# Kernel optimization log

Hardware: AMD Instinct MI355X
Metric: run time of the kernel (lower is better)

Reference implementation:

```python
import jax, jax.numpy as jnp
import numpy as np


def _layernorm(x, g, b, eps=1e-5):
    m = x.mean(-1, keepdims=True)
    v = ((x - m) ** 2).mean(-1, keepdims=True)
    return (x - m) * jax.lax.rsqrt(v + eps) * g + b


def setup_inputs() -> dict:
    key = jax.random.key(0)
    ks = jax.random.split(key, 12)
    B, V, E, N = 8, 64, 512, 32          # batch, num_vars, embed(=input_dim), num_samples
    L, H, D, M, R = 4, 8, 64, 1024, 128  # layers, heads, head_dim, mlp_dim, resolution
    HD = H * D
    s = 0.02
    return {
        "flow_encoded": jax.random.normal(ks[0], (B, V, E), jnp.float32),
        "W_shift": s * jax.random.normal(ks[1], (E, HD), jnp.float32),
        "b_shift": jnp.zeros((HD,), jnp.float32),
        "Wk": s * jax.random.normal(ks[2], (L, H, E, D), jnp.float32),
        "bk": jnp.zeros((L, H, D), jnp.float32),
        "Wv": s * jax.random.normal(ks[3], (L, H, E, D), jnp.float32),
        "bv": jnp.zeros((L, H, D), jnp.float32),
        "ln1_g": jnp.ones((L, HD), jnp.float32),
        "ln1_b": jnp.zeros((L, HD), jnp.float32),
        "W1": s * jax.random.normal(ks[4], (L, HD, M), jnp.float32),
        "b1": jnp.zeros((L, M), jnp.float32),
        "W2": s * jax.random.normal(ks[5], (L, M, M), jnp.float32),
        "b2": jnp.zeros((L, M), jnp.float32),
        "W3": s * jax.random.normal(ks[6], (L, M, HD), jnp.float32),
        "b3": jnp.zeros((L, HD), jnp.float32),
        "ln2_g": jnp.ones((L, HD), jnp.float32),
        "ln2_b": jnp.zeros((L, HD), jnp.float32),
        "W_dist": s * jax.random.normal(ks[7], (HD, R), jnp.float32),
        "b_dist": jnp.zeros((R,), jnp.float32),
        "num_samples": N,
    }


def _forward_logits(flow_encoded, W_shift, b_shift, Wk, bk, Wv, bv,
                    ln1_g, ln1_b, W1, b1, W2, b2, W3, b3, ln2_g, ln2_b,
                    W_dist, b_dist, num_samples):
    B, V, E = flow_encoded.shape
    L, H, _, D = Wk.shape
    HD = H * D
    # history keys/values: all heads in one einsum (replaces per-head nn.Linear loop)
    keys = jnp.einsum('bve,lhed->lbhvd', flow_encoded, Wk) + bk[:, None, :, None, :]
    vals = jnp.einsum('bve,lhed->lbhvd', flow_encoded, Wv) + bv[:, None, :, None, :]
    # queries per (var, sample); vectorized over vars (outer loop in source is independent)
    att = flow_encoded @ W_shift + b_shift                      # [B, V, HD]
    att = jnp.broadcast_to(att[:, :, None, :], (B, V, num_samples, HD))
    scale = D ** -0.5
    for l in range(L):
        q = att.reshape(B, V, num_samples, H, D)
        scores = jnp.einsum('bvnhd,bhwd->bvnhw', q, keys[l]) * scale
        w = jax.nn.softmax(scores, axis=-1)
        a = jnp.einsum('bvnhw,bhwd->bvnhd', w, vals[l]).reshape(B, V, num_samples, HD)
        att = _layernorm(att + a, ln1_g[l], ln1_b[l])
        h = jax.nn.relu(att @ W1[l] + b1[l])
        h = jax.nn.relu(h @ W2[l] + b2[l])
        h = h @ W3[l] + b3[l]
        att = _layernorm(att + h, ln2_g[l], ln2_b[l])
    return att @ W_dist + b_dist                                # [B, V, N, R]


def reference(flow_encoded, W_shift, b_shift, Wk, bk, Wv, bv,
              ln1_g, ln1_b, W1, b1, W2, b2, W3, b3, ln2_g, ln2_b,
              W_dist, b_dist, num_samples):
    logits = _forward_logits(flow_encoded, W_shift, b_shift, Wk, bk, Wv, bv,
                             ln1_g, ln1_b, W1, b1, W2, b2, W3, b3, ln2_g, ln2_b,
                             W_dist, b_dist, num_samples)
    R = b_dist.shape[0]
    k = jax.random.key(1)
    idx = jax.random.categorical(jax.random.fold_in(k, 0), logits, axis=-1)  # multinomial(1)
    u = jax.random.uniform(jax.random.fold_in(k, 1), idx.shape, jnp.float32)
    samples = (idx.astype(jnp.float32) + u) / R                 # [B, V, N]
    return samples
```

## Files before the change

### kernel.cpp

```cpp
#include <hip/hip_runtime.h>
#include <hip/hip_bf16.h>
#include <math.h>

constexpr int B  = 8,  V = 64, E = 512, NS = 32;
constexpr int L  = 4,  H = 8,  D = 64,  M  = 1024, R = 128;
constexpr int HD = H * D;
constexpr int ROWS  = B * V;
constexpr int SROWS = ROWS * NS;
constexpr int KVN = 4096;

typedef _Float16 half8 __attribute__((ext_vector_type(8)));
typedef float floatx4 __attribute__((ext_vector_type(4)));

struct TF2 { unsigned a, b; };
__host__ __device__ constexpr unsigned rotl32(unsigned x, int d) {
  return (x << d) | (x >> (32 - d));
}
__host__ __device__ constexpr TF2 threefry(unsigned k0, unsigned k1,
                                           unsigned x0, unsigned x1) {
  unsigned ks2 = k0 ^ k1 ^ 0x1BD11BDAu;
  x0 += k0; x1 += k1;
  const int ra[4] = {13, 15, 26, 6};
  const int rb[4] = {17, 29, 16, 24};
  for (int i = 0; i < 4; i++) { x0 += x1; x1 = rotl32(x1, ra[i]); x1 ^= x0; }
  x0 += k1;  x1 += ks2 + 1u;
  for (int i = 0; i < 4; i++) { x0 += x1; x1 = rotl32(x1, rb[i]); x1 ^= x0; }
  x0 += ks2; x1 += k0 + 2u;
  for (int i = 0; i < 4; i++) { x0 += x1; x1 = rotl32(x1, ra[i]); x1 ^= x0; }
  x0 += k0;  x1 += k1 + 3u;
  for (int i = 0; i < 4; i++) { x0 += x1; x1 = rotl32(x1, rb[i]); x1 ^= x0; }
  x0 += k1;  x1 += ks2 + 4u;
  for (int i = 0; i < 4; i++) { x0 += x1; x1 = rotl32(x1, ra[i]); x1 ^= x0; }
  x0 += ks2; x1 += k0 + 5u;
  return {x0, x1};
}
__device__ __forceinline__ unsigned tf_bits32(unsigned k0, unsigned k1,
                                              unsigned j) {
  TF2 r = threefry(k0, k1, 0u, j);
  return r.a ^ r.b;
}

__device__ __forceinline__ double waveReduceAdd64(double v) {
#pragma unroll
  for (int m = 32; m; m >>= 1) v += __shfl_xor(v, m, 64);
  return v;
}

__device__ __forceinline__ void split16(float v, _Float16& h, _Float16& l) {
  h = (_Float16)v;
  l = (_Float16)((v - (float)h) * 2048.0f);
}

struct WArgs {
  const float* s[7];
  _Float16* h[7];
  _Float16* l[7];
};
__global__ __launch_bounds__(256) void prep_split(
    WArgs a, const float* __restrict__ flow, const float* __restrict__ bk,
    const float* __restrict__ bv, const float* __restrict__ bsh,
    _Float16* __restrict__ fh, _Float16* __restrict__ fl,
    float* __restrict__ kvb) {
  __shared__ float tile[64][65];
  const int bid = blockIdx.x, t = threadIdx.x;
  if (bid < 275) {
    if (bid < 256) {
      const int base = (bid * 256 + t) * 4;
      float4 v = *(const float4*)&flow[base];
      float x[4] = {v.x, v.y, v.z, v.w};
#pragma unroll
      for (int j = 0; j < 4; j++) {
        _Float16 h, l;
        split16(x[j], h, l);
        fh[base + j] = h;
        fl[base + j] = l;
      }
    } else {
      const int idx = (bid - 256) * 256 + t;
      if (idx < KVN + HD) {
        float bb = (idx < 2048) ? bk[idx]
                 : (idx < 4096) ? bv[idx - 2048]
                                : bsh[idx - 4096];
        kvb[idx] = bb;
      }
    }
    return;
  }
  const int WS_OFF[8] = {0, 64, 320, 576, 1088, 2112, 2624, 2640};
  const int WS_K[7] = {512, 512, 512, 512, 1024, 1024, 512};
  const int WS_N[7] = {512, 64, 64, 1024, 1024, 512, 128};
  int wb = bid - 275;
  int mi = 0;
  while (wb >= WS_OFF[mi + 1]) mi++;
  int tt = wb - WS_OFF[mi];
  const int K = WS_K[mi], N = WS_N[mi];
  const int ktiles = K >> 6;
  const int per = ktiles * (N >> 6);
  const int z = tt / per;
  const int rem = tt - z * per;
  const int k0 = (rem % ktiles) * 64, n0 = (rem / ktiles) * 64;
  const size_t moff = (size_t)z * K * N;
  const float* src = a.s[mi] + moff;
  _Float16* dh = a.h[mi] + moff;
  _Float16* dl = a.l[mi] + moff;
#pragma unroll
  for (int i = 0; i < 16; i++) {
    int idx = i * 256 + t, r = idx >> 6, c = idx & 63;
    tile[r][c] = src[(size_t)(k0 + r) * N + n0 + c];
  }
  __syncthreads();
#pragma unroll
  for (int i = 0; i < 16; i++) {
    int idx = i * 256 + t, n = idx >> 6, k = idx & 63;
    float v = tile[k][n];
    _Float16 h, l;
    split16(v, h, l);
    dh[(size_t)(n0 + n) * K + k0 + k] = h;
    dl[(size_t)(n0 + n) * K + k0 + k] = l;
  }
}

#define GEMM64_BODY(Ah, Al, Bh, Bl, K, m0, n0, kbase, kchunk, hh, mid, lds)  \
  {                                                                          \
    const int t = threadIdx.x, lane = t & 63, wave = t >> 6;                 \
    const int KT = (kchunk) >> 5;                                            \
    const int l15w = lane & 15, quadw = lane >> 4;                           \
    const _Float16* srcs[4] = {                                              \
        (Ah) + (size_t)(m0) * (K), (Al) + (size_t)(m0) * (K),                \
        (Bh) + (size_t)(n0) * (K), (Bl) + (size_t)(n0) * (K)};               \
    const _Float16* gsrc =                                                   \
        srcs[wave] + (size_t)l15w * (K) + quadw * 8 + (kbase);               \
    auto stage = [&](int buf, int kt) {                                      \
      _Float16* base = &lds[buf * 8192 + wave * 2048];                       \
      const int koff = kt * 32;                                              \
      _Pragma("unroll") for (int f = 0; f < 4; f++)                          \
          __builtin_amdgcn_global_load_lds(                                  \
              gsrc + (size_t)(f * 16) * (K) + koff, base + f * 512, 16, 0,   \
              0);                                                            \
    };                                                                       \
    const int wm = wave >> 1, wn = wave & 1;                                 \
    stage(0, 0);                                                             \
    __syncthreads();                                                         \
    for (int kt = 0; kt < KT; kt++) {                                        \
      if (kt + 1 < KT) stage((kt + 1) & 1, kt + 1);                          \
      const int bofs = (kt & 1) * 8192;                                      \
      half8 a_h[2], a_l[2], b_h[2], b_l[2];                                  \
      _Pragma("unroll") for (int i = 0; i < 2; i++) {                        \
        const int af = (wm * 2 + i) * 512 + lane * 8;                        \
        const int bf = (wn * 2 + i) * 512 + lane * 8;                        \
        a_h[i] = *(const half8*)&lds[bofs + af];                             \
        a_l[i] = *(const half8*)&lds[bofs + 2048 + af];                      \
        b_h[i] = *(const half8*)&lds[bofs + 4096 + bf];                      \
        b_l[i] = *(const half8*)&lds[bofs + 6144 + bf];                      \
      }                                                                      \
      _Pragma("unroll") for (int i = 0; i < 2; i++)                          \
          _Pragma("unroll") for (int j = 0; j < 2; j++) {                    \
        hh[i][j] = __builtin_amdgcn_mfma_f32_16x16x32_f16(a_h[i], b_h[j],    \
                                                          hh[i][j], 0, 0, 0);\
        mid[i][j] = __builtin_amdgcn_mfma_f32_16x16x32_f16(                  \
            a_h[i], b_l[j], mid[i][j], 0, 0, 0);                             \
        mid[i][j] = __builtin_amdgcn_mfma_f32_16x16x32_f16(                  \
            a_l[i], b_h[j], mid[i][j], 0, 0, 0);                             \
      }                                                                      \
      __syncthreads();                                                       \
    }                                                                        \
  }

#define GEMM_ACC_INIT(hh, mid)                                               \
  floatx4 hh[2][2], mid[2][2];                                               \
  _Pragma("unroll") for (int i = 0; i < 2; i++)                              \
      _Pragma("unroll") for (int j = 0; j < 2; j++) {                        \
    hh[i][j] = (floatx4){0.f, 0.f, 0.f, 0.f};                                \
    mid[i][j] = (floatx4){0.f, 0.f, 0.f, 0.f};                               \
  }

__global__ __launch_bounds__(256) void gemm_kv(
    const _Float16* __restrict__ Ah, const _Float16* __restrict__ Al,
    const _Float16* __restrict__ Bh, const _Float16* __restrict__ Bl,
    const float* __restrict__ kvb, float* __restrict__ kv,
    float* __restrict__ att) {
  __shared__ __align__(16) _Float16 lds[2 * 8192];
  const int n0 = blockIdx.x * 64, m0 = blockIdx.y * 64;
  GEMM_ACC_INIT(hh, mid)
  GEMM64_BODY(Ah, Al, Bh, Bl, 512, m0, n0, 0, 512, hh, mid, lds)
  const int t = threadIdx.x, lane = t & 63, wave = t >> 6;
  const int wm = wave >> 1, wn = wave & 1, quad = lane >> 4, l15 = lane & 15;
#pragma unroll
  for (int i = 0; i < 2; i++)
#pragma unroll
    for (int j = 0; j < 2; j++)
#pragma unroll
      for (int r = 0; r < 4; r++) {
        float v = hh[i][j][r] + mid[i][j][r] * (1.0f / 2048.0f);
        const int m = m0 + (wm * 2 + i) * 16 + quad * 4 + r;
        const int n = n0 + (wn * 2 + j) * 16 + l15;
        v += kvb[n];
        if (n < KVN) kv[(size_t)m * KVN + n] = v;
        else att[(size_t)m * HD + (n - KVN)] = v;
      }
}

__global__ __launch_bounds__(256) void gemm_sp(
    const _Float16* __restrict__ Ah, const _Float16* __restrict__ Al,
    const _Float16* __restrict__ Bh, const _Float16* __restrict__ Bl,
    float* __restrict__ P, int K, int kchunk, int Ndim) {
  __shared__ __align__(16) _Float16 lds[2 * 8192];
  const int n0 = blockIdx.x * 64, m0 = blockIdx.y * 64;
  const int kbase = blockIdx.z * kchunk;
  GEMM_ACC_INIT(hh, mid)
  GEMM64_BODY(Ah, Al, Bh, Bl, K, m0, n0, kbase, kchunk, hh, mid, lds)
  const int t = threadIdx.x, lane = t & 63, wave = t >> 6;
  const int wm = wave >> 1, wn = wave & 1, quad = lane >> 4, l15 = lane & 15;
  float* Pz = P + (size_t)blockIdx.z * ROWS * Ndim;
#pragma unroll
  for (int i = 0; i < 2; i++)
#pragma unroll
    for (int j = 0; j < 2; j++)
#pragma unroll
      for (int r = 0; r < 4; r++) {
        float v = hh[i][j][r] + mid[i][j][r] * (1.0f / 2048.0f);
        const int m = m0 + (wm * 2 + i) * 16 + quad * 4 + r;
        const int n = n0 + (wn * 2 + j) * 16 + l15;
        Pz[(size_t)m * Ndim + n] = v;
      }
}

__global__ __launch_bounds__(256) void gemm_eh(
    const _Float16* __restrict__ Ah, const _Float16* __restrict__ Al,
    const _Float16* __restrict__ Bh, const _Float16* __restrict__ Bl,
    const float* __restrict__ bias, _Float16* __restrict__ Oh,
    _Float16* __restrict__ Ol, int K, int Ndim, int relu) {
  __shared__ __align__(16) _Float16 lds[2 * 8192];
  const int n0 = blockIdx.x * 64, m0 = blockIdx.y * 64;
  GEMM_ACC_INIT(hh, mid)
  GEMM64_BODY(Ah, Al, Bh, Bl, K, m0, n0, 0, K, hh, mid, lds)
  const int t = threadIdx.x, lane = t & 63, wave = t >> 6;
  const int wm = wave >> 1, wn = wave & 1, quad = lane >> 4, l15 = lane & 15;
#pragma unroll
  for (int i = 0; i < 2; i++)
#pragma unroll
    for (int j = 0; j < 2; j++)
#pragma unroll
      for (int r = 0; r < 4; r++) {
        float v = hh[i][j][r] + mid[i][j][r] * (1.0f / 2048.0f);
        const int m = m0 + (wm * 2 + i) * 16 + quad * 4 + r;
        const int n = n0 + (wn * 2 + j) * 16 + l15;
        v += bias[n];
        if (relu) v = fmaxf(v, 0.0f);
        _Float16 h, l;
        split16(v, h, l);
        const size_t id = (size_t)m * Ndim + n;
        Oh[id] = h;
        Ol[id] = l;
      }
}

__global__ __launch_bounds__(256) void gemm_dist(
    const _Float16* __restrict__ Ah, const _Float16* __restrict__ Al,
    const _Float16* __restrict__ Bh, const _Float16* __restrict__ Bl,
    const float* __restrict__ bd, float* __restrict__ logits) {
  __shared__ __align__(16) _Float16 lds[2 * 8192];
  const int n0 = blockIdx.x * 64, m0 = blockIdx.y * 64;
  GEMM_ACC_INIT(hh, mid)
  GEMM64_BODY(Ah, Al, Bh, Bl, 512, m0, n0, 0, 512, hh, mid, lds)
  const int t = threadIdx.x, lane = t & 63, wave = t >> 6;
  const int wm = wave >> 1, wn = wave & 1, quad = lane >> 4, l15 = lane & 15;
#pragma unroll
  for (int i = 0; i < 2; i++)
#pragma unroll
    for (int j = 0; j < 2; j++)
#pragma unroll
      for (int r = 0; r < 4; r++) {
        float v = hh[i][j][r] + mid[i][j][r] * (1.0f / 2048.0f);
        const int m = m0 + (wm * 2 + i) * 16 + quad * 4 + r;
        const int n = n0 + (wn * 2 + j) * 16 + l15;
        logits[(size_t)m * R + n] = v + bd[n];
      }
}

__device__ __forceinline__ void attn_core(
    float* __restrict__ att, _Float16* __restrict__ att_h,
    _Float16* __restrict__ att_l, const float* __restrict__ kv,
    const float* __restrict__ g, const float* __restrict__ bb, int l, int row,
    float q0, float q1) {
  __shared__ float q[HD];
  __shared__ float sp[HD];
  __shared__ double rb[8];
  const int t = threadIdx.x;
  const int b_ = row >> 6;
  q[t] = q0;
  q[t + 256] = q1;
  __syncthreads();
#pragma unroll
  for (int rep = 0; rep < 2; rep++) {
    int idx = t + rep * 256;
    int h = idx >> 6, w = idx & 63;
    const float* kp = kv + (size_t)(b_ * 64 + w) * KVN + (l * 8 + h) * 64;
    const float* qp = q + h * D;
    double s = 0.0;
#pragma unroll 8
    for (int d = 0; d < 64; d++) s += (double)qp[d] * (double)kp[d];
    sp[idx] = (float)s * 0.125f;
  }
  __syncthreads();
  {
    int h = t >> 5, w0 = t & 31;
    float s0 = sp[h * 64 + w0], s1 = sp[h * 64 + w0 + 32];
    float mx = fmaxf(s0, s1);
#pragma unroll
    for (int m = 16; m; m >>= 1) mx = fmaxf(mx, __shfl_xor(mx, m, 32));
    float e0 = expf(s0 - mx), e1 = expf(s1 - mx);
    double sm = (double)e0 + (double)e1;
#pragma unroll
    for (int m = 16; m; m >>= 1) sm += __shfl_xor(sm, m, 32);
    sp[h * 64 + w0]      = (float)((double)e0 / sm);
    sp[h * 64 + w0 + 32] = (float)((double)e1 / sm);
  }
  __syncthreads();
  float x[2];
#pragma unroll
  for (int rep = 0; rep < 2; rep++) {
    int idx = t + rep * 256;
    int h = idx >> 6, d = idx & 63;
    const float* vp =
        kv + (size_t)(b_ * 64) * KVN + 2048 + (l * 8 + h) * 64 + d;
    const float* pp = sp + h * 64;
    double acc = 0.0;
#pragma unroll 8
    for (int w = 0; w < 64; w++)
      acc += (double)pp[w] * (double)vp[(size_t)w * KVN];
    x[rep] = q[idx] + (float)acc;
  }
  double s1 = (double)x[0] + (double)x[1];
  double s2 = (double)x[0] * (double)x[0] + (double)x[1] * (double)x[1];
  s1 = waveReduceAdd64(s1);
  s2 = waveReduceAdd64(s2);
  const int wid = t >> 6, lane = t & 63;
  if (lane == 0) { rb[wid] = s1; rb[4 + wid] = s2; }
  __syncthreads();
  double S1 = rb[0] + rb[1] + rb[2] + rb[3];
  double S2 = rb[4] + rb[5] + rb[6] + rb[7];
  double mean = S1 / (double)HD;
  double var  = S2 / (double)HD - mean * mean;
  double inv  = 1.0 / sqrt(var + (double)1e-5f);
  float y0 =
      (float)(((double)x[0] - mean) * inv * (double)g[t] + (double)bb[t]);
  float y1 = (float)(((double)x[1] - mean) * inv * (double)g[t + 256] +
                     (double)bb[t + 256]);
  att[row * HD + t] = y0;
  att[row * HD + 256 + t] = y1;
  _Float16 h0, l0, h1v, l1v;
  split16(y0, h0, l0);
  split16(y1, h1v, l1v);
  att_h[row * HD + t] = h0;
  att_l[row * HD + t] = l0;
  att_h[row * HD + 256 + t] = h1v;
  att_l[row * HD + 256 + t] = l1v;
}

__global__ __launch_bounds__(256) void attn_kernel(
    float* __restrict__ att, _Float16* __restrict__ att_h,
    _Float16* __restrict__ att_l, const float* __restrict__ kv,
    const float* __restrict__ g, const float* __restrict__ bb, int l) {
  const int t = threadIdx.x, row = blockIdx.x;
  float q0 = att[row * HD + t];
  float q1 = att[row * HD + 256 + t];
  attn_core(att, att_h, att_l, kv, g, bb, l, row, q0, q1);
}

__global__ __launch_bounds__(256) void epi_ln_attn(
    float* __restrict__ att, _Float16* __restrict__ att_h,
    _Float16* __restrict__ att_l, const float* __restrict__ P,
    const float* __restrict__ b3, const float* __restrict__ g2,
    const float* __restrict__ bb2, const float* __restrict__ kv,
    const float* __restrict__ g1, const float* __restrict__ bb1, int next_l,
    int kz) {
  __shared__ double rb[8];
  const int t = threadIdx.x, row = blockIdx.x;
  const size_t MN = (size_t)ROWS * HD;
  const size_t id0 = (size_t)row * HD + t;
  float h0 = 0.0f, h1s = 0.0f;
  for (int z = 0; z < kz; z++) {
    h0 += P[z * MN + id0];
    h1s += P[z * MN + id0 + 256];
  }
  h0 += b3[t];
  h1s += b3[t + 256];
  float x0 = att[id0] + h0;
  float x1 = att[id0 + 256] + h1s;
  double s1 = (double)x0 + (double)x1;
  double s2 = (double)x0 * (double)x0 + (double)x1 * (double)x1;
  s1 = waveReduceAdd64(s1);
  s2 = waveReduceAdd64(s2);
  const int wid = t >> 6, lane = t & 63;
  if (lane == 0) { rb[wid] = s1; rb[4 + wid] = s2; }
  __syncthreads();
  double S1 = rb[0] + rb[1] + rb[2] + rb[3];
  double S2 = rb[4] + rb[5] + rb[6] + rb[7];
  double mean = S1 / (double)HD;
  double var  = S2 / (double)HD - mean * mean;
  double inv  = 1.0 / sqrt(var + (double)1e-5f);
  float y0 =
      (float)(((double)x0 - mean) * inv * (double)g2[t] + (double)bb2[t]);
  float y1 = (float)(((double)x1 - mean) * inv * (double)g2[t + 256] +
                     (double)bb2[t + 256]);
  if (next_l < 0) {
    att[id0] = y0;
    att[id0 + 256] = y1;
    _Float16 hh0, ll0, hh1, ll1;
    split16(y0, hh0, ll0);
    split16(y1, hh1, ll1);
    att_h[id0] = hh0;
    att_l[id0] = ll0;
    att_h[id0 + 256] = hh1;
    att_l[id0 + 256] = ll1;
  } else {
    __syncthreads();
    attn_core(att, att_h, att_l, kv, g1, bb1, next_l, row, y0, y1);
  }
}

__global__ __launch_bounds__(256) void sample_kernel(
    const float* __restrict__ logits, float* __restrict__ out) {
  constexpr TF2 KC = threefry(0u, 1u, 0u, 0u);
  constexpr TF2 KU = threefry(0u, 1u, 0u, 1u);
  const int lane = threadIdx.x & 63;
  const int wid = threadIdx.x >> 6;
  const int row = blockIdx.x * 4 + wid;
  const float* lrow = logits + (row >> 5) * R;
  float bvv = -1e30f;
  int bi = 0;
#pragma unroll
  for (int rep = 0; rep < 2; rep++) {
    int r = lane + rep * 64;
    unsigned j = (unsigned)row * (unsigned)R + (unsigned)r;
    unsigned bits = tf_bits32(KC.a, KC.b, j);
    float f = __uint_as_float((bits >> 9) | 0x3f800000u) - 1.0f;
    float u = fmaxf(f, 1.17549435e-38f);
    float gv = -logf(-logf(u));
    float v = lrow[r] + gv;
    if (v > bvv) { bvv = v; bi = r; }
  }
#pragma unroll
  for (int m = 32; m; m >>= 1) {
    float ov = __shfl_xor(bvv, m, 64);
    int oi = __shfl_xor(bi, m, 64);
    if (ov > bvv || (ov == bvv && oi < bi)) { bvv = ov; bi = oi; }
  }
  if (lane == 0) {
    unsigned ub = tf_bits32(KU.a, KU.b, (unsigned)row);
    float u = __uint_as_float((ub >> 9) | 0x3f800000u) - 1.0f;
    out[row] = ((float)bi + u) * (1.0f / 128.0f);
  }
}

extern "C" void kernel_launch(void* const* d_in, const int* in_sizes, int n_in,
                              void* d_out, int out_size, void* d_ws,
                              size_t ws_size, hipStream_t stream) {
  (void)in_sizes; (void)n_in; (void)out_size; (void)ws_size;
  const float* flow = (const float*)d_in[0];
  const float* Wsh  = (const float*)d_in[1];
  const float* bsh  = (const float*)d_in[2];
  const float* Wk   = (const float*)d_in[3];
  const float* bk   = (const float*)d_in[4];
  const float* Wv   = (const float*)d_in[5];
  const float* bv   = (const float*)d_in[6];
  const float* ln1g = (const float*)d_in[7];
  const float* ln1b = (const float*)d_in[8];
  const float* W1   = (const float*)d_in[9];
  const float* b1   = (const float*)d_in[10];
  const float* W2   = (const float*)d_in[11];
  const float* b2   = (const float*)d_in[12];
  const float* W3   = (const float*)d_in[13];
  const float* b3   = (const float*)d_in[14];
  const float* ln2g = (const float*)d_in[15];
  const float* ln2b = (const float*)d_in[16];
  const float* Wd   = (const float*)d_in[17];
  const float* bd   = (const float*)d_in[18];

  float* ws = (float*)d_ws;
  float* kv     = ws;
  float* att    = kv + ROWS * KVN;
  float* logits = att + ROWS * HD;
  float* kvb    = logits + ROWS * R;
  float* P      = kvb + 4608;
  _Float16* hp = (_Float16*)(P + 4718592);
  _Float16* flow_h = hp;            hp += 262144;
  _Float16* flow_l = hp;            hp += 262144;
  _Float16* BKV_h  = hp;            hp += 4608 * 512;
  _Float16* BKV_l  = hp;            hp += 4608 * 512;
  _Float16* W1_h   = hp;            hp += 2097152;
  _Float16* W1_l   = hp;            hp += 2097152;
  _Float16* W2_h   = hp;            hp += 4194304;
  _Float16* W2_l   = hp;            hp += 4194304;
  _Float16* W3_h   = hp;            hp += 2097152;
  _Float16* W3_l   = hp;            hp += 2097152;
  _Float16* Wd_h   = hp;            hp += 65536;
  _Float16* Wd_l   = hp;            hp += 65536;
  _Float16* att_h  = hp;            hp += 262144;
  _Float16* att_l  = hp;            hp += 262144;
  _Float16* h1_h   = hp;            hp += 524288;
  _Float16* h1_l   = hp;            hp += 524288;
  _Float16* h2_h   = hp;            hp += 524288;
  _Float16* h2_l   = hp;            hp += 524288;

  WArgs wa;
  wa.s[0] = Wsh; wa.h[0] = BKV_h + 4096 * 512; wa.l[0] = BKV_l + 4096 * 512;
  wa.s[1] = Wk;  wa.h[1] = BKV_h;              wa.l[1] = BKV_l;
  wa.s[2] = Wv;  wa.h[2] = BKV_h + 2048 * 512; wa.l[2] = BKV_l + 2048 * 512;
  wa.s[3] = W1;  wa.h[3] = W1_h;  wa.l[3] = W1_l;
  wa.s[4] = W2;  wa.h[4] = W2_h;  wa.l[4] = W2_l;
  wa.s[5] = W3;  wa.h[5] = W3_h;  wa.l[5] = W3_l;
  wa.s[6] = Wd;  wa.h[6] = Wd_h;  wa.l[6] = Wd_l;
  prep_split<<<2915, 256, 0, stream>>>(wa, flow, bk, bv, bsh, flow_h, flow_l,
                                       kvb);

  gemm_kv<<<dim3(72, 8), 256, 0, stream>>>(flow_h, flow_l, BKV_h, BKV_l, kvb,
                                           kv, att);
  attn_kernel<<<ROWS, 256, 0, stream>>>(att, att_h, att_l, kv, ln1g, ln1b, 0);

  for (int l = 0; l < L; l++) {
    gemm_eh<<<dim3(16, 8), 256, 0, stream>>>(
        att_h, att_l, W1_h + (size_t)l * 524288, W1_l + (size_t)l * 524288,
        b1 + l * M, h1_h, h1_l, 512, M, 1);
    gemm_eh<<<dim3(16, 8), 256, 0, stream>>>(
        h1_h, h1_l, W2_h + (size_t)l * 1048576, W2_l + (size_t)l * 1048576,
        b2 + l * M, h2_h, h2_l, 1024, M, 1);
    gemm_sp<<<dim3(8, 8, 4), 256, 0, stream>>>(
        h2_h, h2_l, W3_h + (size_t)l * 524288, W3_l + (size_t)l * 524288, P,
        1024, 256, HD);
    const int nl = (l + 1 < L) ? (l + 1) : -1;
    epi_ln_attn<<<ROWS, 256, 0, stream>>>(
        att, att_h, att_l, P, b3 + l * HD, ln2g + l * HD, ln2b + l * HD, kv,
        ln1g + (nl < 0 ? 0 : nl) * HD, ln1b + (nl < 0 ? 0 : nl) * HD, nl, 4);
  }
  gemm_dist<<<dim3(2, 8), 256, 0, stream>>>(att_h, att_l, Wd_h, Wd_l, bd,
                                            logits);
  sample_kernel<<<SROWS / 4, 256, 0, stream>>>(logits, (float*)d_out);
}
```

Measured before the change: 459.6 us.

## Split-K the MLP GEMMs with last-block atomic reduction epilogue

The W1 and W2 GEMMs, which previously launched only 128 blocks each, now use split-K (4 and 8 chunks). Each block writes fp32 partials, and the last block per tile (found with an atomic counter) sums them, adds bias, applies ReLU and splits to fp16 hi/lo. The W3 GEMM also goes from 4 to 8 K-chunks, with the LN epilogue reducing 8 partials. The aim is better CU occupancy on the small grids, at the cost of extra partial-sum traffic, fences and atomics.

```diff
diff --git a/kernel.cpp b/kernel.cpp
--- a/kernel.cpp
+++ b/kernel.cpp
@@ -60,7 +60,7 @@
     WArgs a, const float* __restrict__ flow, const float* __restrict__ bk,
     const float* __restrict__ bv, const float* __restrict__ bsh,
     _Float16* __restrict__ fh, _Float16* __restrict__ fl,
-    float* __restrict__ kvb) {
+    float* __restrict__ kvb, int* __restrict__ cnt) {
   __shared__ float tile[64][65];
   const int bid = blockIdx.x, t = threadIdx.x;
   if (bid < 275) {
@@ -82,6 +82,8 @@
                  : (idx < 4096) ? bv[idx - 2048]
                                 : bsh[idx - 4096];
         kvb[idx] = bb;
+      } else if (t < 128) {
+        cnt[t] = 0;
       }
     }
     return;
@@ -174,6 +176,21 @@
     mid[i][j] = (floatx4){0.f, 0.f, 0.f, 0.f};                               \
   }
 
+#define PARTIAL_EPI(Pz, Ndim, m0, n0, hh, mid)                               \
+  {                                                                          \
+    const int t = threadIdx.x, lane = t & 63, wave = t >> 6;                 \
+    const int wm = wave >> 1, wn = wave & 1, quad = lane >> 4,               \
+              l15 = lane & 15;                                               \
+    _Pragma("unroll") for (int i = 0; i < 2; i++)                            \
+        _Pragma("unroll") for (int j = 0; j < 2; j++)                        \
+            _Pragma("unroll") for (int r = 0; r < 4; r++) {                  \
+      float v = hh[i][j][r] + mid[i][j][r] * (1.0f / 2048.0f);               \
+      const int m = (m0) + (wm * 2 + i) * 16 + quad * 4 + r;                 \
+      const int n = (n0) + (wn * 2 + j) * 16 + l15;                          \
+      (Pz)[(size_t)m * (Ndim) + n] = v;                                      \
+    }                                                                        \
+  }
+
 __global__ __launch_bounds__(256) void gemm_kv(
     const _Float16* __restrict__ Ah, const _Float16* __restrict__ Al,
     const _Float16* __restrict__ Bh, const _Float16* __restrict__ Bl,
@@ -209,50 +226,51 @@
   const int kbase = blockIdx.z * kchunk;
   GEMM_ACC_INIT(hh, mid)
   GEMM64_BODY(Ah, Al, Bh, Bl, K, m0, n0, kbase, kchunk, hh, mid, lds)
-  const int t = threadIdx.x, lane = t & 63, wave = t >> 6;
-  const int wm = wave >> 1, wn = wave & 1, quad = lane >> 4, l15 = lane & 15;
   float* Pz = P + (size_t)blockIdx.z * ROWS * Ndim;
-#pragma unroll
-  for (int i = 0; i < 2; i++)
-#pragma unroll
-    for (int j = 0; j < 2; j++)
-#pragma unroll
-      for (int r = 0; r < 4; r++) {
-        float v = hh[i][j][r] + mid[i][j][r] * (1.0f / 2048.0f);
-        const int m = m0 + (wm * 2 + i) * 16 + quad * 4 + r;
-        const int n = n0 + (wn * 2 + j) * 16 + l15;
-        Pz[(size_t)m * Ndim + n] = v;
-      }
-}
-
-__global__ __launch_bounds__(256) void gemm_eh(
+  PARTIAL_EPI(Pz, Ndim, m0, n0, hh, mid)
+}
+
+__global__ __launch_bounds__(256) void gemm_f(
     const _Float16* __restrict__ Ah, const _Float16* __restrict__ Al,
     const _Float16* __restrict__ Bh, const _Float16* __restrict__ Bl,
-    const float* __restrict__ bias, _Float16* __restrict__ Oh,
-    _Float16* __restrict__ Ol, int K, int Ndim, int relu) {
+    float* __restrict__ P, const float* __restrict__ bias,
+    _Float16* __restrict__ Oh, _Float16* __restrict__ Ol,
+    int* __restrict__ cnt, int K, int kchunk, int Ndim, int kz) {
   __shared__ __align__(16) _Float16 lds[2 * 8192];
+  __shared__ int isLast;
   const int n0 = blockIdx.x * 64, m0 = blockIdx.y * 64;
+  const int kbase = blockIdx.z * kchunk;
   GEMM_ACC_INIT(hh, mid)
-  GEMM64_BODY(Ah, Al, Bh, Bl, K, m0, n0, 0, K, hh, mid, lds)
-  const int t = threadIdx.x, lane = t & 63, wave = t >> 6;
-  const int wm = wave >> 1, wn = wave & 1, quad = lane >> 4, l15 = lane & 15;
-#pragma unroll
-  for (int i = 0; i < 2; i++)
-#pragma unroll
-    for (int j = 0; j < 2; j++)
-#pragma unroll
-      for (int r = 0; r < 4; r++) {
-        float v = hh[i][j][r] + mid[i][j][r] * (1.0f / 2048.0f);
-        const int m = m0 + (wm * 2 + i) * 16 + quad * 4 + r;
-        const int n = n0 + (wn * 2 + j) * 16 + l15;
-        v += bias[n];
-        if (relu) v = fmaxf(v, 0.0f);
-        _Float16 h, l;
-        split16(v, h, l);
-        const size_t id = (size_t)m * Ndim + n;
-        Oh[id] = h;
-        Ol[id] = l;
-      }
+  GEMM64_BODY(Ah, Al, Bh, Bl, K, m0, n0, kbase, kchunk, hh, mid, lds)
+  float* Pz = P + (size_t)blockIdx.z * ROWS * Ndim;
+  PARTIAL_EPI(Pz, Ndim, m0, n0, hh, mid)
+  __threadfence();
+  __syncthreads();
+  const int tile = blockIdx.y * gridDim.x + blockIdx.x;
+  if (threadIdx.x == 0) {
+    int old = atomicAdd(&cnt[tile], 1);
+    isLast = (old == kz - 1) ? 1 : 0;
+  }
+  __syncthreads();
+  if (isLast) {
+    __threadfence();
+    const size_t MN = (size_t)ROWS * Ndim;
+#pragma unroll
+    for (int ii = 0; ii < 16; ii++) {
+      const int idx = ii * 256 + threadIdx.x;
+      const int m = m0 + (idx >> 6), n = n0 + (idx & 63);
+      const size_t id = (size_t)m * Ndim + n;
+      float v = 0.0f;
+      for (int z = 0; z < kz; z++) v += P[z * MN + id];
+      v += bias[n];
+      v = fmaxf(v, 0.0f);
+      _Float16 h, l;
+      split16(v, h, l);
+      Oh[id] = h;
+      Ol[id] = l;
+    }
+    if (threadIdx.x == 0) cnt[tile] = 0;
+  }
 }
 
 __global__ __launch_bounds__(256) void gemm_dist(
@@ -483,7 +501,8 @@
   float* att    = kv + ROWS * KVN;
   float* logits = att + ROWS * HD;
   float* kvb    = logits + ROWS * R;
-  float* P      = kvb + 4608;
+  int*   cnt    = (int*)(kvb + 4608);
+  float* P      = kvb + 4608 + 128;
   _Float16* hp = (_Float16*)(P + 4718592);
   _Float16* flow_h = hp;            hp += 262144;
   _Float16* flow_l = hp;            hp += 262144;
@@ -513,26 +532,26 @@
   wa.s[5] = W3;  wa.h[5] = W3_h;  wa.l[5] = W3_l;
   wa.s[6] = Wd;  wa.h[6] = Wd_h;  wa.l[6] = Wd_l;
   prep_split<<<2915, 256, 0, stream>>>(wa, flow, bk, bv, bsh, flow_h, flow_l,
-                                       kvb);
+                                       kvb, cnt);
 
   gemm_kv<<<dim3(72, 8), 256, 0, stream>>>(flow_h, flow_l, BKV_h, BKV_l, kvb,
                                            kv, att);
   attn_kernel<<<ROWS, 256, 0, stream>>>(att, att_h, att_l, kv, ln1g, ln1b, 0);
 
   for (int l = 0; l < L; l++) {
-    gemm_eh<<<dim3(16, 8), 256, 0, stream>>>(
-        att_h, att_l, W1_h + (size_t)l * 524288, W1_l + (size_t)l * 524288,
-        b1 + l * M, h1_h, h1_l, 512, M, 1);
-    gemm_eh<<<dim3(16, 8), 256, 0, stream>>>(
-        h1_h, h1_l, W2_h + (size_t)l * 1048576, W2_l + (size_t)l * 1048576,
-        b2 + l * M, h2_h, h2_l, 1024, M, 1);
-    gemm_sp<<<dim3(8, 8, 4), 256, 0, stream>>>(
+    gemm_f<<<dim3(16, 8, 4), 256, 0, stream>>>(
+        att_h, att_l, W1_h + (size_t)l * 524288, W1_l + (size_t)l * 524288, P,
+        b1 + l * M, h1_h, h1_l, cnt, 512, 128, M, 4);
+    gemm_f<<<dim3(16, 8, 8), 256, 0, stream>>>(
+        h1_h, h1_l, W2_h + (size_t)l * 1048576, W2_l + (size_t)l * 1048576, P,
+        b2 + l * M, h2_h, h2_l, cnt, 1024, 128, M, 8);
+    gemm_sp<<<dim3(8, 8, 8), 256, 0, stream>>>(
         h2_h, h2_l, W3_h + (size_t)l * 524288, W3_l + (size_t)l * 524288, P,
-        1024, 256, HD);
+        1024, 128, HD);
     const int nl = (l + 1 < L) ? (l + 1) : -1;
     epi_ln_attn<<<ROWS, 256, 0, stream>>>(
         att, att_h, att_l, P, b3 + l * HD, ln2g + l * HD, ln2b + l * HD, kv,
-        ln1g + (nl < 0 ? 0 : nl) * HD, ln1b + (nl < 0 ? 0 : nl) * HD, nl, 4);
+        ln1g + (nl < 0 ? 0 : nl) * HD, ln1b + (nl < 0 ? 0 : nl) * HD, nl, 8);
   }
   gemm_dist<<<dim3(2, 8), 256, 0, stream>>>(att_h, att_l, Wd_h, Wd_l, bd,
                                             logits);
```

Result: slower. 1.323 ms (+187.7%).
